# Optimization experiments

Measured on AMD Instinct MI355X. Metric: run time of the kernel, lower is better.

Reference implementation:

```python
import jax, jax.numpy as jnp
import numpy as np

THRESH = 0.6


def _build_targets(targets, anchors, nH, nW, nA):
    # Vectorized replacement of the torch per-target python double loop.
    B, T, _ = targets.shape
    valid = jnp.sum(targets, axis=-1) != 0            # [B,T] skip all-zero rows
    label = targets[..., 0].astype(jnp.int32)
    gx = targets[..., 1] * nW
    gy = targets[..., 2] * nH
    gw = targets[..., 3] * nW
    gh = targets[..., 4] * nH
    gi = jnp.floor(gx).astype(jnp.int32)              # int(gx)
    gj = jnp.floor(gy).astype(jnp.int32)              # int(gy)
    aw, ah = anchors[:, 0], anchors[:, 1]             # [A]
    # IoU of (0,0,gw,gh) vs (0,0,aw,ah): co-centered boxes
    inter = jnp.minimum(gw[..., None], aw) * jnp.minimum(gh[..., None], ah)
    union = gw[..., None] * gh[..., None] + aw * ah - inter
    iou = inter / union                               # [B,T,A]
    best = jnp.argmax(iou, axis=-1)                   # [B,T]
    b_idx = jnp.broadcast_to(jnp.arange(B)[:, None], (B, T))
    safe_b = jnp.where(valid, b_idx, B)               # OOB batch idx -> scatter dropped
    a_all = jnp.broadcast_to(jnp.arange(nA), (B, T, nA))
    hb = jnp.where(valid[..., None] & (iou > THRESH), b_idx[..., None], B)

    Z = lambda: jnp.zeros((B, nA, nH, nW), jnp.float32)
    conf_mask = jnp.ones((B, nA, nH, nW), jnp.float32)
    conf_mask = conf_mask.at[hb, a_all, gj[..., None], gi[..., None]].set(0.0)
    conf_mask = conf_mask.at[safe_b, best, gj, gi].set(1.0)
    mask = Z().at[safe_b, best, gj, gi].set(1.0)
    tx = Z().at[safe_b, best, gj, gi].set(gx - jnp.floor(gx))
    ty = Z().at[safe_b, best, gj, gi].set(gy - jnp.floor(gy))
    tw = Z().at[safe_b, best, gj, gi].set(jnp.log(gw / aw[best] + 1e-16))
    th = Z().at[safe_b, best, gj, gi].set(jnp.log(gh / ah[best] + 1e-16))
    tlabel = jnp.zeros((B, nA, nH, nW), jnp.int32).at[safe_b, best, gj, gi].set(label)
    return mask, conf_mask, tx, ty, tw, th, tlabel


def reference(x, targets, anchors):
    B = x.shape[0]
    nA = anchors.shape[0]
    nH, nW = x.shape[2], x.shape[3]
    attrs = x.shape[1] // nA                          # 7 + num_classes
    pred = x.reshape(B, nA, attrs, nH, nW).transpose(0, 1, 3, 4, 2)  # [B,A,H,W,attrs]
    px = jax.nn.sigmoid(pred[..., 0])
    py = jax.nn.sigmoid(pred[..., 1])
    pw = pred[..., 2]
    ph = pred[..., 3]
    pconf = jax.nn.sigmoid(pred[..., 6])
    pcls = jax.nn.sigmoid(pred[..., 7:])              # [B,A,H,W,C]

    mask, conf_mask, tx, ty, tw, th, tlabel = _build_targets(targets, anchors, nH, nW, nA)

    n_obj = jnp.sum(mask)
    mmean = lambda d: jnp.sum(d * mask) / n_obj       # masked MSE (size_average)
    loss_x = mmean((px - tx) ** 2)
    loss_y = mmean((py - ty) ** 2)
    loss_w = mmean((pw - tw) ** 2)
    loss_h = mmean((ph - th) ** 2)

    tconf = mask
    p = jnp.clip(pconf, 1e-7, 1.0 - 1e-7)
    bce_el = -(tconf * jnp.log(p) + (1.0 - tconf) * jnp.log1p(-p))
    noobj = conf_mask * (1.0 - mask)                  # conf_mask - mask (byte sub)
    loss_conf = jnp.sum(bce_el * noobj) / jnp.sum(noobj) + jnp.sum(bce_el * mask) / n_obj

    # CrossEntropy on sigmoided class scores (faithful to the torch quirk)
    logp = jax.nn.log_softmax(pcls, axis=-1)
    ce = -jnp.take_along_axis(logp, tlabel[..., None], axis=-1)[..., 0]
    loss_cls = (1.0 / B) * jnp.sum(ce * mask) / n_obj

    return loss_x + loss_y + loss_w + loss_h + loss_conf + loss_cls


def setup_inputs() -> dict:
    key = jax.random.key(0)
    k1, k2, k3 = jax.random.split(key, 3)
    B, nA, nC, nH, nW, T = 8, 5, 8, 192, 192, 50
    x = jax.random.normal(k1, (B, nA * (7 + nC), nH, nW), jnp.float32)
    # targets: (label, cx, cy, w, h); coords normalized in (0,1)
    coords = jax.random.uniform(k2, (B, T, 4), jnp.float32, 1e-3, 0.999)
    labels = jax.random.randint(k3, (B, T, 1), 0, nC).astype(jnp.float32)
    targets = jnp.concatenate([labels, coords], axis=-1)
    anchors = jnp.array([[1.08, 1.19], [3.42, 4.41], [6.63, 11.38],
                         [9.42, 5.11], [16.62, 10.52]], jnp.float32)
    return {"x": x, "targets": targets, "anchors": anchors}
```

## Files before the change

kernel.cpp:

```cpp
#include <hip/hip_runtime.h>
#include <math.h>

#define BB 8
#define NA 5
#define NC 8
#define NH 192
#define NW 192
#define TT 50
#define ATTRS 15
#define THRESH_F 0.6f

#define NTGT (BB * TT)
#define PLANE (NH * NW)
#define BATCH_CELLS (NA * PLANE)
#define NCELLS (BB * BATCH_CELLS)
#define HSZ 4096
#define HEMPTY 0xFFFFFFFFu

#define TICK_OFF 128
#define PART_OFF 192
#define CONF_BLOCKS 360
#define CONF_THREADS 256
#define CONF_TOTAL (CONF_BLOCKS * CONF_THREADS)

struct Rec {
    int cell;
    int label;
    float tx, ty, tw, th;
    int valid;
    int pad;
};

__device__ __forceinline__ float sigmoidf_(float v) {
    return 1.0f / (1.0f + expf(-v));
}

__device__ __forceinline__ float noobj_term(float v) {
    float p = fminf(fmaxf(sigmoidf_(v), 1e-7f), 1.0f - 1e-7f);
    return -log1pf(-p);
}

__global__ __launch_bounds__(512) void build_obj_k(const float* __restrict__ x,
                                                   const float* __restrict__ tgt,
                                                   const float* __restrict__ anchors,
                                                   double* __restrict__ acc,
                                                   unsigned int* __restrict__ ticket) {
    __shared__ Rec srecs[NTGT];
    __shared__ unsigned int hset[HSZ];
    __shared__ double wsum[8][9];
    const int tid = threadIdx.x;

    for (int i = tid; i < HSZ; i += 512) hset[i] = HEMPTY;
    if (tid == 0) *ticket = 0u;
    __syncthreads();

    double corr_b = 0.0, corr_c = 0.0;

    if (tid < NTGT) {
        const int b = tid / TT;
        const float* p = tgt + (size_t)tid * 5;
        float lab = p[0], cx = p[1], cy = p[2], cw = p[3], ch = p[4];
        int valid = ((lab + cx + cy + cw + ch) != 0.0f) ? 1 : 0;
        float gx = cx * NW, gy = cy * NH, gw = cw * NW, gh = ch * NH;
        int gi = min(max((int)floorf(gx), 0), NW - 1);
        int gj = min(max((int)floorf(gy), 0), NH - 1);
        float ious[NA];
        float aw[NA], ah[NA];
        int best = 0; float bi = -1.0f;
        #pragma unroll
        for (int a = 0; a < NA; ++a) {
            aw[a] = anchors[2 * a];
            ah[a] = anchors[2 * a + 1];
            float inter = fminf(gw, aw[a]) * fminf(gh, ah[a]);
            float un = gw * gh + aw[a] * ah[a] - inter;
            float iou = inter / un;
            ious[a] = iou;
            if (iou > bi) { bi = iou; best = a; }
        }
        if (valid) {
            #pragma unroll
            for (int a = 0; a <= NA; ++a) {
                int aa; bool doit;
                if (a < NA) { aa = a; doit = (ious[a] > THRESH_F); }
                else        { aa = best; doit = true; }
                if (!doit) continue;
                unsigned int key = (unsigned int)((b * NA + aa) * PLANE + gj * NW + gi);
                unsigned int h = (key * 2654435761u) & (HSZ - 1);
                while (true) {
                    unsigned int old = atomicCAS(&hset[h], HEMPTY, key);
                    if (old == HEMPTY) {
                        int cb = key / BATCH_CELLS;
                        int cr = key % BATCH_CELLS;
                        int ca = cr / PLANE;
                        int chw = cr % PLANE;
                        float v = x[((size_t)(cb * NA + ca) * ATTRS + 6) * PLANE + chw];
                        corr_b += (double)noobj_term(v);
                        corr_c += 1.0;
                        break;
                    }
                    if (old == key) break;
                    h = (h + 1) & (HSZ - 1);
                }
            }
        }
        Rec r;
        r.valid = valid;
        r.cell = (best * NH + gj) * NW + gi;
        r.label = (int)lab;
        r.tx = gx - floorf(gx);
        r.ty = gy - floorf(gy);
        r.tw = logf(gw / aw[best] + 1e-16f);
        r.th = logf(gh / ah[best] + 1e-16f);
        srecs[tid] = r;
    }
    __syncthreads();

    double v[9];
    #pragma unroll
    for (int k = 0; k < 9; ++k) v[k] = 0.0;
    v[7] = corr_b;
    v[8] = corr_c;

    if (tid < NTGT) {
        Rec r = srecs[tid];
        if (r.valid) {
            const int b = tid / TT, t = tid % TT;
            bool superseded = false;
            for (int t2 = t + 1; t2 < TT; ++t2) {
                Rec r2 = srecs[b * TT + t2];
                if (r2.valid && r2.cell == r.cell) { superseded = true; break; }
            }
            if (!superseded) {
                int a  = r.cell / PLANE;
                int hw = r.cell % PLANE;
                size_t base = ((size_t)(b * NA + a) * ATTRS) * PLANE + hw;
                float v0 = x[base + 0 * PLANE];
                float v1 = x[base + 1 * PLANE];
                float v2 = x[base + 2 * PLANE];
                float v3 = x[base + 3 * PLANE];
                float v6 = x[base + 6 * PLANE];
                float px = sigmoidf_(v0);
                float py = sigmoidf_(v1);
                float pconf = fminf(fmaxf(sigmoidf_(v6), 1e-7f), 1.0f - 1e-7f);
                float c[NC];
                float m = -INFINITY;
                #pragma unroll
                for (int k = 0; k < NC; ++k) {
                    float sv = sigmoidf_(x[base + (size_t)(7 + k) * PLANE]);
                    c[k] = sv;
                    m = fmaxf(m, sv);
                }
                float se = 0.0f;
                #pragma unroll
                for (int k = 0; k < NC; ++k) se += expf(c[k] - m);
                float lse = m + logf(se);
                v[0] = 1.0;
                v[1] = (double)((px - r.tx) * (px - r.tx));
                v[2] = (double)((py - r.ty) * (py - r.ty));
                v[3] = (double)((v2 - r.tw) * (v2 - r.tw));
                v[4] = (double)((v3 - r.th) * (v3 - r.th));
                v[5] = (double)(-logf(pconf));
                v[6] = (double)(lse - c[r.label]);
            }
        }
    }

    #pragma unroll
    for (int k = 0; k < 9; ++k)
        for (int off = 32; off > 0; off >>= 1)
            v[k] += __shfl_down(v[k], off);
    const int lane = tid & 63, wid = tid >> 6;
    if (lane == 0) {
        #pragma unroll
        for (int k = 0; k < 9; ++k) wsum[wid][k] = v[k];
    }
    __syncthreads();
    if (tid == 0) {
        #pragma unroll
        for (int k = 0; k < 9; ++k) {
            double s = 0.0;
            #pragma unroll
            for (int w = 0; w < 8; ++w) s += wsum[w][k];
            acc[k] = s;
        }
    }
}

__global__ __launch_bounds__(256) void conf_fused_k(const float* __restrict__ x,
                                                    const double* __restrict__ acc,
                                                    unsigned int* __restrict__ ticket,
                                                    double* __restrict__ partials,
                                                    float* __restrict__ out) {
    __shared__ double wred[4];
    __shared__ int s_last;
    const int g = blockIdx.x * CONF_THREADS + threadIdx.x;
    double s = 0.0;
    #pragma unroll
    for (int it = 0; it < 4; ++it) {
        int n4 = g + it * CONF_TOTAL;
        int n = n4 * 4;
        int b = n / BATCH_CELLS;
        int rr = n % BATCH_CELLS;
        int a = rr / PLANE;
        int hw = rr % PLANE;
        const float4 v = *reinterpret_cast<const float4*>(
            x + ((size_t)(b * NA + a) * ATTRS + 6) * PLANE + hw);
        s += (double)noobj_term(v.x) + (double)noobj_term(v.y)
           + (double)noobj_term(v.z) + (double)noobj_term(v.w);
    }
    for (int off = 32; off > 0; off >>= 1) s += __shfl_down(s, off);
    const int lane = threadIdx.x & 63, wid = threadIdx.x >> 6;
    if (lane == 0) wred[wid] = s;
    __syncthreads();
    if (threadIdx.x == 0) {
        partials[blockIdx.x] = wred[0] + wred[1] + wred[2] + wred[3];
        __threadfence();
        unsigned int t = atomicAdd(ticket, 1u);
        s_last = (t == CONF_BLOCKS - 1) ? 1 : 0;
    }
    __syncthreads();
    if (!s_last) return;

    __threadfence();
    double sb = 0.0;
    for (int i = threadIdx.x; i < CONF_BLOCKS; i += CONF_THREADS) sb += partials[i];
    for (int off = 32; off > 0; off >>= 1) sb += __shfl_down(sb, off);
    if (lane == 0) wred[wid] = sb;
    __syncthreads();
    if (threadIdx.x == 0) {
        double dense = wred[0] + wred[1] + wred[2] + wred[3];
        double n_obj = acc[0];
        double noobj_b = dense - acc[7];
        double noobj_c = (double)NCELLS - acc[8];
        double loss = (acc[1] + acc[2] + acc[3] + acc[4]) / n_obj
                    + noobj_b / noobj_c
                    + acc[5] / n_obj
                    + (1.0 / (double)BB) * acc[6] / n_obj;
        out[0] = (float)loss;
    }
}

extern "C" void kernel_launch(void* const* d_in, const int* in_sizes, int n_in,
                              void* d_out, int out_size, void* d_ws, size_t ws_size,
                              hipStream_t stream) {
    const float* x       = (const float*)d_in[0];
    const float* tgt     = (const float*)d_in[1];
    const float* anchors = (const float*)d_in[2];

    double* acc          = (double*)d_ws;
    unsigned int* ticket = (unsigned int*)((char*)d_ws + TICK_OFF);
    double* partials     = (double*)((char*)d_ws + PART_OFF);

    build_obj_k<<<1, 512, 0, stream>>>(x, tgt, anchors, acc, ticket);
    conf_fused_k<<<CONF_BLOCKS, CONF_THREADS, 0, stream>>>(x, acc, ticket, partials,
                                                           (float*)d_out);
}
```

Measured before the change: 154.7 us.

## Fuse target-build and dense no-object reduction into one heterogeneous grid

Merges the single-block target/object kernel and the dense confidence reduction kernel into one launch. The last block handles the targets while the other blocks reduce the confidence channel, so the two phases run concurrently instead of serially. All blocks accumulate into workspace with double atomics and a ticket counter, and the final block computes the loss. A hipMemsetAsync is added to zero the workspace, which adds a small extra stream operation, and the double atomicAdds have contention risk.

```diff
diff --git a/kernel.cpp b/kernel.cpp
--- a/kernel.cpp
+++ b/kernel.cpp
@@ -17,11 +17,37 @@
 #define HSZ 4096
 #define HEMPTY 0xFFFFFFFFu
 
-#define TICK_OFF 128
-#define PART_OFF 192
-#define CONF_BLOCKS 360
-#define CONF_THREADS 256
-#define CONF_TOTAL (CONF_BLOCKS * CONF_THREADS)
+#define DENSE_BLOCKS 180
+#define GRID_BLOCKS (DENSE_BLOCKS + 1)
+#define THREADS 512
+#define DENSE_TOTAL (DENSE_BLOCKS * THREADS)
+
+#define TICK_OFF 80
+
+__device__ __forceinline__ float sigmoidf_(float v) {
+    return 1.0f / (1.0f + expf(-v));
+}
+
+__device__ __forceinline__ float noobj_term(float v) {
+    float p = fminf(fmaxf(sigmoidf_(v), 1e-7f), 1.0f - 1e-7f);
+    return -log1pf(-p);
+}
+
+__device__ __forceinline__ double ws_read(double* p) {
+    return atomicAdd(p, 0.0);
+}
+
+__device__ void finalize_(double* ws, float* out) {
+    double n_obj   = ws_read(&ws[0]);
+    double dense   = ws_read(&ws[9]);
+    double noobj_b = dense - ws_read(&ws[7]);
+    double noobj_c = (double)NCELLS - ws_read(&ws[8]);
+    double loss = (ws_read(&ws[1]) + ws_read(&ws[2]) + ws_read(&ws[3]) + ws_read(&ws[4])) / n_obj
+                + noobj_b / noobj_c
+                + ws_read(&ws[5]) / n_obj
+                + (1.0 / (double)BB) * ws_read(&ws[6]) / n_obj;
+    out[0] = (float)loss;
+}
 
 struct Rec {
     int cell;
@@ -31,27 +57,51 @@
     int pad;
 };
 
-__device__ __forceinline__ float sigmoidf_(float v) {
-    return 1.0f / (1.0f + expf(-v));
-}
-
-__device__ __forceinline__ float noobj_term(float v) {
-    float p = fminf(fmaxf(sigmoidf_(v), 1e-7f), 1.0f - 1e-7f);
-    return -log1pf(-p);
-}
-
-__global__ __launch_bounds__(512) void build_obj_k(const float* __restrict__ x,
-                                                   const float* __restrict__ tgt,
-                                                   const float* __restrict__ anchors,
-                                                   double* __restrict__ acc,
-                                                   unsigned int* __restrict__ ticket) {
+__global__ __launch_bounds__(THREADS) void region_loss_k(const float* __restrict__ x,
+                                                         const float* __restrict__ tgt,
+                                                         const float* __restrict__ anchors,
+                                                         double* __restrict__ ws,
+                                                         unsigned int* __restrict__ ticket,
+                                                         float* __restrict__ out) {
     __shared__ Rec srecs[NTGT];
     __shared__ unsigned int hset[HSZ];
     __shared__ double wsum[8][9];
     const int tid = threadIdx.x;
-
-    for (int i = tid; i < HSZ; i += 512) hset[i] = HEMPTY;
-    if (tid == 0) *ticket = 0u;
+    const int bid = blockIdx.x;
+    const int lane = tid & 63, wid = tid >> 6;
+
+    if (bid < DENSE_BLOCKS) {
+        const int g = bid * THREADS + tid;
+        double s = 0.0;
+        #pragma unroll
+        for (int it = 0; it < 4; ++it) {
+            int n4 = g + it * DENSE_TOTAL;
+            int n = n4 * 4;
+            int b = n / BATCH_CELLS;
+            int rr = n % BATCH_CELLS;
+            int a = rr / PLANE;
+            int hw = rr % PLANE;
+            const float4 v = *reinterpret_cast<const float4*>(
+                x + ((size_t)(b * NA + a) * ATTRS + 6) * PLANE + hw);
+            s += (double)noobj_term(v.x) + (double)noobj_term(v.y)
+               + (double)noobj_term(v.z) + (double)noobj_term(v.w);
+        }
+        for (int off = 32; off > 0; off >>= 1) s += __shfl_down(s, off);
+        if (lane == 0) wsum[wid][0] = s;
+        __syncthreads();
+        if (tid == 0) {
+            double bsum = 0.0;
+            #pragma unroll
+            for (int w = 0; w < 8; ++w) bsum += wsum[w][0];
+            atomicAdd(&ws[9], bsum);
+            __threadfence();
+            unsigned int t = atomicAdd(ticket, 1u);
+            if (t == GRID_BLOCKS - 1) finalize_(ws, out);
+        }
+        return;
+    }
+
+    for (int i = tid; i < HSZ; i += THREADS) hset[i] = HEMPTY;
     __syncthreads();
 
     double corr_b = 0.0, corr_c = 0.0;
@@ -169,7 +219,6 @@
     for (int k = 0; k < 9; ++k)
         for (int off = 32; off > 0; off >>= 1)
             v[k] += __shfl_down(v[k], off);
-    const int lane = tid & 63, wid = tid >> 6;
     if (lane == 0) {
         #pragma unroll
         for (int k = 0; k < 9; ++k) wsum[wid][k] = v[k];
@@ -181,62 +230,11 @@
             double s = 0.0;
             #pragma unroll
             for (int w = 0; w < 8; ++w) s += wsum[w][k];
-            acc[k] = s;
-        }
-    }
-}
-
-__global__ __launch_bounds__(256) void conf_fused_k(const float* __restrict__ x,
-                                                    const double* __restrict__ acc,
-                                                    unsigned int* __restrict__ ticket,
-                                                    double* __restrict__ partials,
-                                                    float* __restrict__ out) {
-    __shared__ double wred[4];
-    __shared__ int s_last;
-    const int g = blockIdx.x * CONF_THREADS + threadIdx.x;
-    double s = 0.0;
-    #pragma unroll
-    for (int it = 0; it < 4; ++it) {
-        int n4 = g + it * CONF_TOTAL;
-        int n = n4 * 4;
-        int b = n / BATCH_CELLS;
-        int rr = n % BATCH_CELLS;
-        int a = rr / PLANE;
-        int hw = rr % PLANE;
-        const float4 v = *reinterpret_cast<const float4*>(
-            x + ((size_t)(b * NA + a) * ATTRS + 6) * PLANE + hw);
-        s += (double)noobj_term(v.x) + (double)noobj_term(v.y)
-           + (double)noobj_term(v.z) + (double)noobj_term(v.w);
-    }
-    for (int off = 32; off > 0; off >>= 1) s += __shfl_down(s, off);
-    const int lane = threadIdx.x & 63, wid = threadIdx.x >> 6;
-    if (lane == 0) wred[wid] = s;
-    __syncthreads();
-    if (threadIdx.x == 0) {
-        partials[blockIdx.x] = wred[0] + wred[1] + wred[2] + wred[3];
+            atomicAdd(&ws[k], s);
+        }
         __threadfence();
         unsigned int t = atomicAdd(ticket, 1u);
-        s_last = (t == CONF_BLOCKS - 1) ? 1 : 0;
-    }
-    __syncthreads();
-    if (!s_last) return;
-
-    __threadfence();
-    double sb = 0.0;
-    for (int i = threadIdx.x; i < CONF_BLOCKS; i += CONF_THREADS) sb += partials[i];
-    for (int off = 32; off > 0; off >>= 1) sb += __shfl_down(sb, off);
-    if (lane == 0) wred[wid] = sb;
-    __syncthreads();
-    if (threadIdx.x == 0) {
-        double dense = wred[0] + wred[1] + wred[2] + wred[3];
-        double n_obj = acc[0];
-        double noobj_b = dense - acc[7];
-        double noobj_c = (double)NCELLS - acc[8];
-        double loss = (acc[1] + acc[2] + acc[3] + acc[4]) / n_obj
-                    + noobj_b / noobj_c
-                    + acc[5] / n_obj
-                    + (1.0 / (double)BB) * acc[6] / n_obj;
-        out[0] = (float)loss;
+        if (t == GRID_BLOCKS - 1) finalize_(ws, out);
     }
 }
 
@@ -247,11 +245,11 @@
     const float* tgt     = (const float*)d_in[1];
     const float* anchors = (const float*)d_in[2];
 
-    double* acc          = (double*)d_ws;
+    double* ws           = (double*)d_ws;
     unsigned int* ticket = (unsigned int*)((char*)d_ws + TICK_OFF);
-    double* partials     = (double*)((char*)d_ws + PART_OFF);
-
-    build_obj_k<<<1, 512, 0, stream>>>(x, tgt, anchors, acc, ticket);
-    conf_fused_k<<<CONF_BLOCKS, CONF_THREADS, 0, stream>>>(x, acc, ticket, partials,
-                                                           (float*)d_out);
-}
+
+    hipMemsetAsync(d_ws, 0, 96, stream);
+
+    region_loss_k<<<GRID_BLOCKS, THREADS, 0, stream>>>(x, tgt, anchors, ws, ticket,
+                                                       (float*)d_out);
+}
```

New measurement: 140.2 us. 9.4% less time.
